# Kernel optimization log

Hardware: AMD Instinct MI355X
Metric: run time of the kernel (lower is better)

The kernel has to match this reference:

```python
import jax, jax.numpy as jnp
import numpy as np

B, T, C, H, DH = 4, 2048, 1024, 16, 64  # batch, seq (block_size), n_embd, heads, head_size


def setup_inputs() -> dict:
    key = jax.random.key(0)
    ks = jax.random.split(key, 6)
    x = jax.random.normal(ks[0], (B, T, C), dtype=jnp.float32)
    init = 0.02
    Wq = jax.random.normal(ks[1], (H, C, DH), dtype=jnp.float32) * init
    Wk = jax.random.normal(ks[2], (H, C, DH), dtype=jnp.float32) * init
    Wv = jax.random.normal(ks[3], (H, C, DH), dtype=jnp.float32) * init
    Wp = jax.random.normal(ks[4], (H * DH, C), dtype=jnp.float32) * init
    bp = jnp.zeros((C,), dtype=jnp.float32)
    return {"x": x, "Wq": Wq, "Wk": Wk, "Wv": Wv, "Wp": Wp, "bp": bp}


def reference(x, Wq, Wk, Wv, Wp, bp):
    Bb, Tt, Cc = x.shape
    # per-head projections, vectorized over heads (original loops in Python)
    q = jnp.einsum('btc,hcd->bhtd', x, Wq)
    k = jnp.einsum('btc,hcd->bhtd', x, Wk)
    v = jnp.einsum('btc,hcd->bhtd', x, Wv)
    # NOTE: original scales by rsqrt(C) where C is the INPUT embed dim, not head_size
    scale = 1.0 / jnp.sqrt(jnp.asarray(Cc, dtype=x.dtype))
    wei = jnp.einsum('bhtd,bhsd->bhts', q, k) * scale  # [B,H,T,T]
    causal = jnp.tril(jnp.ones((Tt, Tt), dtype=bool))
    wei = jnp.where(causal, wei, -jnp.inf)
    wei = jax.nn.softmax(wei, axis=-1)
    out = jnp.einsum('bhts,bhsd->bhtd', wei, v)  # [B,H,T,DH]
    # concat heads along feature axis (head h -> slice h*DH:(h+1)*DH)
    out = out.transpose(0, 2, 1, 3).reshape(Bb, Tt, -1)  # [B,T,H*DH]
    out = out @ Wp + bp  # output projection to n_embd
    return out
```

## Files before the change

kernel.cpp:

```cpp
#include <hip/hip_runtime.h>

#define TSEQ 2048
#define CDIM 1024
#define NH 16
#define DH 64
#define NB 4

typedef __bf16 bf16x8 __attribute__((ext_vector_type(8)));
typedef float f32x4 __attribute__((ext_vector_type(4)));

#define QSCALE 0.04508422f

static __device__ __forceinline__ ushort f2bf(float f) {
  unsigned u = __float_as_uint(f);
  unsigned r = u + 0x7fffu + ((u >> 16) & 1u);
  return (ushort)(r >> 16);
}

static __device__ __forceinline__ uint cvtpk(float lo, float hi) {
  uint r;
  asm("v_cvt_pk_bf16_f32 %0, %1, %2" : "=v"(r) : "v"(lo), "v"(hi));
  return r;
}

static __device__ __forceinline__ void gload_lds16(const void* g, void* ldsbase) {
  __builtin_amdgcn_global_load_lds((const __attribute__((address_space(1))) void*)g,
                                   (__attribute__((address_space(3))) void*)ldsbase,
                                   16, 0, 0);
}

__global__ void cvt_x_kernel(const float4* __restrict__ src, ushort4* __restrict__ dst, int n4) {
  int i = blockIdx.x * blockDim.x + threadIdx.x;
  if (i >= n4) return;
  float4 f = src[i];
  ushort4 o;
  o.x = f2bf(f.x); o.y = f2bf(f.y); o.z = f2bf(f.z); o.w = f2bf(f.w);
  dst[i] = o;
}

__global__ void transpose_cvt_all(const float* __restrict__ Wq, const float* __restrict__ Wk,
                                  const float* __restrict__ Wv, const float* __restrict__ Wp,
                                  ushort* __restrict__ wall, ushort* __restrict__ wpT) {
  __shared__ float tile[32][33];
  const int z = blockIdx.z;
  const float* s; ushort* d; int Cc, c0, r0;
  if (z < 3) {
    const int head = blockIdx.x >> 1;
    s = (z == 0 ? Wq : z == 1 ? Wk : Wv) + (size_t)head * CDIM * DH;
    d = wall + ((size_t)z << 20) + (size_t)head * CDIM * DH;
    Cc = DH; c0 = (blockIdx.x & 1) * 32; r0 = blockIdx.y * 32;
  } else {
    s = Wp; d = wpT; Cc = CDIM; c0 = blockIdx.x * 32; r0 = blockIdx.y * 32;
  }
  const int tx = threadIdx.x, ty = threadIdx.y;
  for (int i = ty; i < 32; i += 8)
    tile[i][tx] = s[(size_t)(r0 + i) * Cc + c0 + tx];
  __syncthreads();
  for (int i = ty; i < 32; i += 8)
    d[(size_t)(c0 + i) * CDIM + r0 + tx] = f2bf(tile[tx][i]);
}

template <int MODE>
__global__ __launch_bounds__(256) void gemm_kernel(
    const ushort* __restrict__ A, const ushort* __restrict__ Bt,
    const float* __restrict__ bp, float* __restrict__ fout,
    ushort* __restrict__ qb, ushort* __restrict__ kb, ushort* __restrict__ vTb) {
  __shared__ ushort lds[16384];
  const int tid = threadIdx.x, w = tid >> 6, l = tid & 63;
  const int nwg = gridDim.x;
  const int bid = blockIdx.x;
  const int wgid = (bid & 7) * (nwg >> 3) + (bid >> 3);
  const int NT = (MODE == 0) ? 24 : 8;
  const int nt = wgid % NT, mt = wgid / NT;
  const int wr = w >> 1, wc = w & 1;
  const int srw = l >> 2;
  const int sck = l & 3;
  const int scol = (sck ^ ((srw >> 1) & 3)) * 8;
  const int g = l >> 4;
  char* ldsb = (char*)lds;

  f32x4 acc[4][4] = {};

  const ushort* Arow = A + ((size_t)mt * 128) * CDIM;
  const ushort* Brow = Bt + ((size_t)nt * 128) * CDIM;

#pragma unroll
  for (int i = 0; i < 4; ++i) {
    int ch = w * 4 + i;
    const ushort* src = (ch < 8) ? Arow + (size_t)(ch * 16 + srw) * CDIM + scol
                                 : Brow + (size_t)((ch - 8) * 16 + srw) * CDIM + scol;
    gload_lds16(src, ldsb + ch * 1024);
  }

  for (int k0 = 0; k0 < CDIM; k0 += 32) {
    const int bsel = (k0 >> 5) & 1;
    char* base = ldsb + bsel * 16384;
    __syncthreads();
    if (k0 + 32 < CDIM) {
      char* nb = ldsb + (bsel ^ 1) * 16384;
#pragma unroll
      for (int i = 0; i < 4; ++i) {
        int ch = w * 4 + i;
        const ushort* src = (ch < 8)
            ? Arow + (size_t)(ch * 16 + srw) * CDIM + k0 + 32 + scol
            : Brow + (size_t)((ch - 8) * 16 + srw) * CDIM + k0 + 32 + scol;
        gload_lds16(src, nb + ch * 1024);
      }
    }
    bf16x8 af[4];
#pragma unroll
    for (int fm = 0; fm < 4; ++fm) {
      int row = wr * 64 + fm * 16 + (l & 15);
      af[fm] = *(const bf16x8*)(base + row * 64 + ((g ^ ((row >> 1) & 3)) << 4));
    }
#pragma unroll
    for (int fn = 0; fn < 4; ++fn) {
      int n = wc * 64 + fn * 16 + (l & 15);
      bf16x8 bfr = *(const bf16x8*)(base + 8192 + n * 64 + ((g ^ ((n >> 1) & 3)) << 4));
#pragma unroll
      for (int fm = 0; fm < 4; ++fm)
        acc[fm][fn] = __builtin_amdgcn_mfma_f32_16x16x32_bf16(af[fm], bfr, acc[fm][fn], 0, 0, 0);
    }
  }

#pragma unroll
  for (int fm = 0; fm < 4; ++fm) {
#pragma unroll
    for (int fn = 0; fn < 4; ++fn) {
      const int gr0 = mt * 128 + wr * 64 + fm * 16 + (l >> 4) * 4;
      const int gc = nt * 128 + wc * 64 + fn * 16 + (l & 15);
      if (MODE == 1) {
        float bias = bp[gc];
#pragma unroll
        for (int r = 0; r < 4; ++r)
          fout[(size_t)(gr0 + r) * CDIM + gc] = acc[fm][fn][r] + bias;
      } else {
        const int sel = gc >> 10, h = (gc >> 6) & 15, d = gc & 63;
        const int bh = (gr0 >> 11) * NH + h, tl = gr0 & 2047;
        if (sel == 2) {
          ushort4 pk;
          pk.x = f2bf(acc[fm][fn][0]); pk.y = f2bf(acc[fm][fn][1]);
          pk.z = f2bf(acc[fm][fn][2]); pk.w = f2bf(acc[fm][fn][3]);
          *(ushort4*)(vTb + ((size_t)bh * DH + d) * TSEQ + tl) = pk;
        } else if (sel == 0) {
#pragma unroll
          for (int r = 0; r < 4; ++r)
            qb[((size_t)bh * TSEQ + tl + r) * DH + d] = f2bf(acc[fm][fn][r] * QSCALE);
        } else {
#pragma unroll
          for (int r = 0; r < 4; ++r)
            kb[((size_t)bh * TSEQ + tl + r) * DH + d] = f2bf(acc[fm][fn][r]);
        }
      }
    }
  }
}

__global__ __launch_bounds__(256, 3) void attn_kernel(
    const ushort* __restrict__ qb, const ushort* __restrict__ kb,
    const ushort* __restrict__ vTb, ushort* __restrict__ aob) {
  __shared__ ushort lds[16384];
  char* ldsb = (char*)lds;
  const int tid = threadIdx.x, w = tid >> 6, l = tid & 63;
  const int id = blockIdx.x;
  const int bh = (id & 7) * 8 + ((id >> 3) & 7);
  const int qt = 15 - (id >> 6);
  const int q0 = qt * 128;
  const int nt = 2 * (qt + 1);
  const int b = bh >> 4, h = bh & 15;
  const int g = l >> 4, q = l & 15;
  const int srow = l >> 3;
  const int scol = (((l & 7) ^ srow) << 3);
  const int adrA = ((l & 16) << 1 | q) << 2;
  const int adrB = adrA + 64;
  const bool hi32 = (l & 32) != 0;

  bf16x8 qf[2][2];
#pragma unroll
  for (int qs = 0; qs < 2; ++qs) {
    const ushort* qrow = qb + ((size_t)bh * TSEQ + q0 + w * 32 + qs * 16 + q) * DH;
    qf[qs][0] = *(const bf16x8*)(qrow + 8 * g);
    qf[qs][1] = *(const bf16x8*)(qrow + 32 + 8 * g);
  }

  float m[2] = {0.f, 0.f}, lsum[2] = {0.f, 0.f};
  f32x4 o[4][2] = {};

#pragma unroll
  for (int i = 0; i < 4; ++i) {
    int ch = w * 4 + i;
    if (ch < 8)
      gload_lds16(kb + ((size_t)bh * TSEQ + ch * 8 + srow) * DH + scol, ldsb + ch * 1024);
    else {
      int d = (ch - 8) * 8 + srow;
      gload_lds16(vTb + ((size_t)bh * DH + d) * TSEQ + scol, ldsb + 16384 + (ch - 8) * 1024);
    }
  }

#pragma unroll 1
  for (int j = 0; j < nt; ++j) {
    __syncthreads();
    const int cbuf = j & 1;
    if (j + 1 < nt) {
      const int kvn = (j + 1) * 64, nb = (j + 1) & 1;
#pragma unroll
      for (int i = 0; i < 4; ++i) {
        int ch = w * 4 + i;
        if (ch < 8)
          gload_lds16(kb + ((size_t)bh * TSEQ + kvn + ch * 8 + srow) * DH + scol,
                      ldsb + nb * 8192 + ch * 1024);
        else {
          int d = (ch - 8) * 8 + srow;
          gload_lds16(vTb + ((size_t)bh * DH + d) * TSEQ + kvn + scol,
                      ldsb + 16384 + nb * 8192 + (ch - 8) * 1024);
        }
      }
    }
    char* Kb = ldsb + cbuf * 8192;
    char* Vb = ldsb + 16384 + cbuf * 8192;

    f32x4 s[4][2] = {};
    __builtin_amdgcn_s_setprio(1);
#pragma unroll
    for (int ks = 0; ks < 2; ++ks)
#pragma unroll
      for (int fn = 0; fn < 4; ++fn) {
        int n = fn * 16 + q;
        int cbb = (ks * 64 + 16 * g) ^ ((n & 7) << 4);
        bf16x8 kf = *(const bf16x8*)(Kb + n * 128 + cbb);
        s[fn][0] = __builtin_amdgcn_mfma_f32_16x16x32_bf16(kf, qf[0][ks], s[fn][0], 0, 0, 0);
        s[fn][1] = __builtin_amdgcn_mfma_f32_16x16x32_bf16(kf, qf[1][ks], s[fn][1], 0, 0, 0);
      }
    __builtin_amdgcn_s_setprio(0);

    if (j >= nt - 2) {
#pragma unroll
      for (int qs = 0; qs < 2; ++qs) {
        int rowloc = q0 + w * 32 + qs * 16 + q - j * 64;
#pragma unroll
        for (int fn = 0; fn < 4; ++fn)
#pragma unroll
          for (int r = 0; r < 4; ++r)
            if (fn * 16 + 4 * g + r > rowloc) s[fn][qs][r] = -1e30f;
      }
    }

    float vmx[2];
#pragma unroll
    for (int qs = 0; qs < 2; ++qs) {
      float v = fmaxf(fmaxf(fmaxf(s[0][qs][0], s[0][qs][1]), fmaxf(s[0][qs][2], s[0][qs][3])),
                      fmaxf(fmaxf(s[1][qs][0], s[1][qs][1]), fmaxf(s[1][qs][2], s[1][qs][3])));
      v = fmaxf(v, fmaxf(fmaxf(fmaxf(s[2][qs][0], s[2][qs][1]), fmaxf(s[2][qs][2], s[2][qs][3])),
                         fmaxf(fmaxf(s[3][qs][0], s[3][qs][1]), fmaxf(s[3][qs][2], s[3][qs][3]))));
      vmx[qs] = v;
    }
    if (__any(fmaxf(vmx[0] - m[0], vmx[1] - m[1]) > 8.f)) {
      float fc[2];
#pragma unroll
      for (int qs = 0; qs < 2; ++qs) {
        float v = vmx[qs];
        v = fmaxf(v, __shfl_xor(v, 16));
        v = fmaxf(v, __shfl_xor(v, 32));
        float mn = fmaxf(m[qs], v);
        fc[qs] = __builtin_amdgcn_exp2f(m[qs] - mn);
        m[qs] = mn; lsum[qs] *= fc[qs];
      }
#pragma unroll
      for (int r = 0; r < 4; ++r) {
        float f0 = __shfl(fc[0], (l & 0x30) | (4 * g + r), 64);
        float f1 = __shfl(fc[1], (l & 0x30) | (4 * g + r), 64);
#pragma unroll
        for (int fn = 0; fn < 4; ++fn) { o[fn][0][r] *= f0; o[fn][1][r] *= f1; }
      }
    }

    uint D[2][4][2];
#pragma unroll
    for (int qs = 0; qs < 2; ++qs) {
      float rs = 0.f;
#pragma unroll
      for (int fn = 0; fn < 4; ++fn) {
        float p0 = __builtin_amdgcn_exp2f(s[fn][qs][0] - m[qs]);
        float p1 = __builtin_amdgcn_exp2f(s[fn][qs][1] - m[qs]);
        float p2 = __builtin_amdgcn_exp2f(s[fn][qs][2] - m[qs]);
        float p3 = __builtin_amdgcn_exp2f(s[fn][qs][3] - m[qs]);
        rs += (p0 + p1) + (p2 + p3);
        D[qs][fn][0] = cvtpk(p0, p1);
        D[qs][fn][1] = cvtpk(p2, p3);
      }
      lsum[qs] += rs;
    }

#pragma unroll
    for (int ksg = 0; ksg < 2; ++ksg) {
      union { uint u[4]; bf16x8 v; } P[2];
#pragma unroll
      for (int qs = 0; qs < 2; ++qs) {
        uint t0a = __builtin_amdgcn_ds_bpermute(adrA, (int)D[qs][2 * ksg][0]);
        uint t0b = __builtin_amdgcn_ds_bpermute(adrA, (int)D[qs][2 * ksg + 1][0]);
        uint t1a = __builtin_amdgcn_ds_bpermute(adrA, (int)D[qs][2 * ksg][1]);
        uint t1b = __builtin_amdgcn_ds_bpermute(adrA, (int)D[qs][2 * ksg + 1][1]);
        uint t2a = __builtin_amdgcn_ds_bpermute(adrB, (int)D[qs][2 * ksg][0]);
        uint t2b = __builtin_amdgcn_ds_bpermute(adrB, (int)D[qs][2 * ksg + 1][0]);
        uint t3a = __builtin_amdgcn_ds_bpermute(adrB, (int)D[qs][2 * ksg][1]);
        uint t3b = __builtin_amdgcn_ds_bpermute(adrB, (int)D[qs][2 * ksg + 1][1]);
        P[qs].u[0] = hi32 ? t0b : t0a;
        P[qs].u[1] = hi32 ? t1b : t1a;
        P[qs].u[2] = hi32 ? t2b : t2a;
        P[qs].u[3] = hi32 ? t3b : t3a;
      }
      __builtin_amdgcn_s_setprio(1);
#pragma unroll
      for (int fn = 0; fn < 4; ++fn) {
        int n = fn * 16 + q;
        int cbb = (ksg * 64 + 16 * g) ^ ((n & 7) << 4);
        bf16x8 vf = *(const bf16x8*)(Vb + n * 128 + cbb);
        o[fn][0] = __builtin_amdgcn_mfma_f32_16x16x32_bf16(P[0].v, vf, o[fn][0], 0, 0, 0);
        o[fn][1] = __builtin_amdgcn_mfma_f32_16x16x32_bf16(P[1].v, vf, o[fn][1], 0, 0, 0);
      }
      __builtin_amdgcn_s_setprio(0);
    }
  }

#pragma unroll
  for (int qs = 0; qs < 2; ++qs) {
    float tot = lsum[qs];
    tot += __shfl_xor(tot, 16);
    tot += __shfl_xor(tot, 32);
    float inv = 1.f / tot;
#pragma unroll
    for (int r = 0; r < 4; ++r) {
      float invq = __shfl(inv, (l & 0x30) | (4 * g + r), 64);
      int t = q0 + w * 32 + qs * 16 + 4 * g + r;
#pragma unroll
      for (int fn = 0; fn < 4; ++fn) {
        int d = fn * 16 + q;
        aob[((size_t)b * TSEQ + t) * (NH * DH) + h * DH + d] = f2bf(o[fn][qs][r] * invq);
      }
    }
  }
}

extern "C" void kernel_launch(void* const* d_in, const int* in_sizes, int n_in,
                              void* d_out, int out_size, void* d_ws, size_t ws_size,
                              hipStream_t stream) {
  (void)in_sizes; (void)n_in; (void)out_size; (void)ws_size;
  const float* x  = (const float*)d_in[0];
  const float* Wq = (const float*)d_in[1];
  const float* Wk = (const float*)d_in[2];
  const float* Wv = (const float*)d_in[3];
  const float* Wp = (const float*)d_in[4];
  const float* bp = (const float*)d_in[5];
  float* out = (float*)d_out;
  char* ws = (char*)d_ws;

  ushort* xb  = (ushort*)(ws);
  ushort* wall = (ushort*)(ws + (16ull << 20));
  ushort* wpT = (ushort*)(ws + (22ull << 20));
  ushort* qb  = (ushort*)(ws + (24ull << 20));
  ushort* kb  = (ushort*)(ws + (40ull << 20));
  ushort* vTb = (ushort*)(ws + (56ull << 20));
  ushort* aob = (ushort*)(ws + (72ull << 20));

  cvt_x_kernel<<<(NB * TSEQ * CDIM / 4 + 255) / 256, 256, 0, stream>>>(
      (const float4*)x, (ushort4*)xb, NB * TSEQ * CDIM / 4);
  transpose_cvt_all<<<dim3(32, 32, 4), dim3(32, 8), 0, stream>>>(Wq, Wk, Wv, Wp, wall, wpT);

  gemm_kernel<0><<<dim3(64 * 24), 256, 0, stream>>>(xb, wall, nullptr, nullptr, qb, kb, vTb);
  attn_kernel<<<dim3(1024), 256, 0, stream>>>(qb, kb, vTb, aob);
  gemm_kernel<1><<<dim3(64 * 8), 256, 0, stream>>>(aob, wpT, bp, out, nullptr, nullptr, nullptr);
}
```

Before: 176.0 us.

## Triple-buffer LDS with explicit vmcnt waits in GEMM and attention kernels

```diff
diff --git a/kernel.cpp b/kernel.cpp
--- a/kernel.cpp
+++ b/kernel.cpp
@@ -65,7 +65,7 @@
     const ushort* __restrict__ A, const ushort* __restrict__ Bt,
     const float* __restrict__ bp, float* __restrict__ fout,
     ushort* __restrict__ qb, ushort* __restrict__ kb, ushort* __restrict__ vTb) {
-  __shared__ ushort lds[16384];
+  __shared__ ushort lds[24576];
   const int tid = threadIdx.x, w = tid >> 6, l = tid & 63;
   const int nwg = gridDim.x;
   const int bid = blockIdx.x;
@@ -91,36 +91,49 @@
                                  : Brow + (size_t)((ch - 8) * 16 + srw) * CDIM + scol;
     gload_lds16(src, ldsb + ch * 1024);
   }
-
+  asm volatile("" ::: "memory");
+#pragma unroll
+  for (int i = 0; i < 4; ++i) {
+    int ch = w * 4 + i;
+    const ushort* src = (ch < 8) ? Arow + (size_t)(ch * 16 + srw) * CDIM + 32 + scol
+                                 : Brow + (size_t)((ch - 8) * 16 + srw) * CDIM + 32 + scol;
+    gload_lds16(src, ldsb + 16384 + ch * 1024);
+  }
+
+  char* bc = ldsb;
+  char* b1 = ldsb + 16384;
+  char* b2 = ldsb + 32768;
+#pragma unroll 1
   for (int k0 = 0; k0 < CDIM; k0 += 32) {
-    const int bsel = (k0 >> 5) & 1;
-    char* base = ldsb + bsel * 16384;
-    __syncthreads();
-    if (k0 + 32 < CDIM) {
-      char* nb = ldsb + (bsel ^ 1) * 16384;
+    if (k0 + 32 < CDIM) asm volatile("s_waitcnt vmcnt(4)" ::: "memory");
+    else                asm volatile("s_waitcnt vmcnt(0)" ::: "memory");
+    __builtin_amdgcn_s_barrier();
+    __builtin_amdgcn_sched_barrier(0);
+    if (k0 + 64 < CDIM) {
 #pragma unroll
       for (int i = 0; i < 4; ++i) {
         int ch = w * 4 + i;
         const ushort* src = (ch < 8)
-            ? Arow + (size_t)(ch * 16 + srw) * CDIM + k0 + 32 + scol
-            : Brow + (size_t)((ch - 8) * 16 + srw) * CDIM + k0 + 32 + scol;
-        gload_lds16(src, nb + ch * 1024);
+            ? Arow + (size_t)(ch * 16 + srw) * CDIM + k0 + 64 + scol
+            : Brow + (size_t)((ch - 8) * 16 + srw) * CDIM + k0 + 64 + scol;
+        gload_lds16(src, b2 + ch * 1024);
       }
     }
     bf16x8 af[4];
 #pragma unroll
     for (int fm = 0; fm < 4; ++fm) {
       int row = wr * 64 + fm * 16 + (l & 15);
-      af[fm] = *(const bf16x8*)(base + row * 64 + ((g ^ ((row >> 1) & 3)) << 4));
+      af[fm] = *(const bf16x8*)(bc + row * 64 + ((g ^ ((row >> 1) & 3)) << 4));
     }
 #pragma unroll
     for (int fn = 0; fn < 4; ++fn) {
       int n = wc * 64 + fn * 16 + (l & 15);
-      bf16x8 bfr = *(const bf16x8*)(base + 8192 + n * 64 + ((g ^ ((n >> 1) & 3)) << 4));
+      bf16x8 bfr = *(const bf16x8*)(bc + 8192 + n * 64 + ((g ^ ((n >> 1) & 3)) << 4));
 #pragma unroll
       for (int fm = 0; fm < 4; ++fm)
         acc[fm][fn] = __builtin_amdgcn_mfma_f32_16x16x32_bf16(af[fm], bfr, acc[fm][fn], 0, 0, 0);
     }
+    char* t = bc; bc = b1; b1 = b2; b2 = t;
   }
 
 #pragma unroll
@@ -159,7 +172,7 @@
 __global__ __launch_bounds__(256, 3) void attn_kernel(
     const ushort* __restrict__ qb, const ushort* __restrict__ kb,
     const ushort* __restrict__ vTb, ushort* __restrict__ aob) {
-  __shared__ ushort lds[16384];
+  __shared__ ushort lds[24576];
   char* ldsb = (char*)lds;
   const int tid = threadIdx.x, w = tid >> 6, l = tid & 63;
   const int id = blockIdx.x;
@@ -193,31 +206,47 @@
       gload_lds16(kb + ((size_t)bh * TSEQ + ch * 8 + srow) * DH + scol, ldsb + ch * 1024);
     else {
       int d = (ch - 8) * 8 + srow;
-      gload_lds16(vTb + ((size_t)bh * DH + d) * TSEQ + scol, ldsb + 16384 + (ch - 8) * 1024);
-    }
-  }
-
+      gload_lds16(vTb + ((size_t)bh * DH + d) * TSEQ + scol, ldsb + 24576 + (ch - 8) * 1024);
+    }
+  }
+  asm volatile("" ::: "memory");
+#pragma unroll
+  for (int i = 0; i < 4; ++i) {
+    int ch = w * 4 + i;
+    if (ch < 8)
+      gload_lds16(kb + ((size_t)bh * TSEQ + 64 + ch * 8 + srow) * DH + scol,
+                  ldsb + 8192 + ch * 1024);
+    else {
+      int d = (ch - 8) * 8 + srow;
+      gload_lds16(vTb + ((size_t)bh * DH + d) * TSEQ + 64 + scol,
+                  ldsb + 24576 + 8192 + (ch - 8) * 1024);
+    }
+  }
+
+  int oc = 0, o1 = 8192, o2 = 16384;
 #pragma unroll 1
   for (int j = 0; j < nt; ++j) {
-    __syncthreads();
-    const int cbuf = j & 1;
-    if (j + 1 < nt) {
-      const int kvn = (j + 1) * 64, nb = (j + 1) & 1;
+    if (j + 1 < nt) asm volatile("s_waitcnt vmcnt(4)" ::: "memory");
+    else            asm volatile("s_waitcnt vmcnt(0)" ::: "memory");
+    __builtin_amdgcn_s_barrier();
+    __builtin_amdgcn_sched_barrier(0);
+    if (j + 2 < nt) {
+      const int kvn = (j + 2) * 64;
 #pragma unroll
       for (int i = 0; i < 4; ++i) {
         int ch = w * 4 + i;
         if (ch < 8)
           gload_lds16(kb + ((size_t)bh * TSEQ + kvn + ch * 8 + srow) * DH + scol,
-                      ldsb + nb * 8192 + ch * 1024);
+                      ldsb + o2 + ch * 1024);
         else {
           int d = (ch - 8) * 8 + srow;
           gload_lds16(vTb + ((size_t)bh * DH + d) * TSEQ + kvn + scol,
-                      ldsb + 16384 + nb * 8192 + (ch - 8) * 1024);
+                      ldsb + 24576 + o2 + (ch - 8) * 1024);
         }
       }
     }
-    char* Kb = ldsb + cbuf * 8192;
-    char* Vb = ldsb + 16384 + cbuf * 8192;
+    char* Kb = ldsb + oc;
+    char* Vb = ldsb + 24576 + oc;
 
     f32x4 s[4][2] = {};
     __builtin_amdgcn_s_setprio(1);
@@ -320,6 +349,7 @@
       }
       __builtin_amdgcn_s_setprio(0);
     }
+    int t = oc; oc = o1; o1 = o2; o2 = t;
   }
 
 #pragma unroll
```

Measured after the change: 182.4 us. +3.7%, slower.

## Replace QKV projection GEMM with 256x256-tile 8-wave triple-buffered kernel

Applied to the files above, without the earlier changes.

```diff
diff --git a/kernel.cpp b/kernel.cpp
--- a/kernel.cpp
+++ b/kernel.cpp
@@ -58,6 +58,138 @@
   __syncthreads();
   for (int i = ty; i < 32; i += 8)
     d[(size_t)(c0 + i) * CDIM + r0 + tx] = f2bf(tile[tx][i]);
+}
+
+__global__ __launch_bounds__(512, 2) void qkv8_kernel(
+    const ushort* __restrict__ A, const ushort* __restrict__ Bt,
+    ushort* __restrict__ qb, ushort* __restrict__ kb, ushort* __restrict__ vTb) {
+  __shared__ ushort lds[49152];
+  char* ldsb = (char*)lds;
+  const int tid = threadIdx.x, w = tid >> 6, l = tid & 63;
+  const int nwg = gridDim.x;
+  const int bid = blockIdx.x;
+  const int wgid = (bid & 7) * (nwg >> 3) + (bid >> 3);
+  const int nt = wgid % 12, mt = wgid / 12;
+  const int wr = w >> 2, wc = w & 3;
+  const int g = l >> 4;
+  const int scc = (l & 3) ^ ((l >> 3) & 3);
+  const int strow = l >> 2;
+
+  f32x4 acc[8][4] = {};
+
+  const ushort* Arow = A + ((size_t)mt * 256) * CDIM;
+  const ushort* Brow = Bt + ((size_t)nt * 256) * CDIM;
+
+#pragma unroll
+  for (int tt = 0; tt < 2; ++tt) {
+    char* sl = ldsb + tt * 32768;
+#pragma unroll
+    for (int i = 0; i < 2; ++i) {
+      int ch = w * 2 + i;
+      gload_lds16(Arow + (size_t)(ch * 16 + strow) * CDIM + tt * 32 + scc * 8, sl + ch * 1024);
+    }
+#pragma unroll
+    for (int i = 0; i < 2; ++i) {
+      int ch = w * 2 + i;
+      gload_lds16(Brow + (size_t)(ch * 16 + strow) * CDIM + tt * 32 + scc * 8,
+                  sl + 16384 + ch * 1024);
+    }
+  }
+  asm volatile("s_waitcnt vmcnt(4)" ::: "memory");
+  __builtin_amdgcn_s_barrier();
+
+  char* sl0 = ldsb;
+  char* sl1 = ldsb + 32768;
+  char* sl2 = ldsb + 65536;
+
+#pragma unroll 1
+  for (int t = 0; t < 32; ++t) {
+    bf16x8 af[4], bf[4];
+#pragma unroll
+    for (int fm = 0; fm < 4; ++fm) {
+      int row = wr * 128 + fm * 16 + (l & 15);
+      af[fm] = *(const bf16x8*)(sl0 + row * 64 + ((g ^ ((row >> 1) & 3)) << 4));
+    }
+#pragma unroll
+    for (int fn = 0; fn < 4; ++fn) {
+      int n = wc * 64 + fn * 16 + (l & 15);
+      bf[fn] = *(const bf16x8*)(sl0 + 16384 + n * 64 + ((g ^ ((n >> 1) & 3)) << 4));
+    }
+    if (t + 2 < 32) {
+#pragma unroll
+      for (int i = 0; i < 2; ++i) {
+        int ch = w * 2 + i;
+        gload_lds16(Arow + (size_t)(ch * 16 + strow) * CDIM + (t + 2) * 32 + scc * 8,
+                    sl2 + ch * 1024);
+      }
+    }
+    __builtin_amdgcn_s_barrier();
+    asm volatile("s_waitcnt lgkmcnt(0)" ::: "memory");
+    __builtin_amdgcn_sched_barrier(0);
+    __builtin_amdgcn_s_setprio(1);
+#pragma unroll
+    for (int fn = 0; fn < 4; ++fn)
+#pragma unroll
+      for (int fm = 0; fm < 4; ++fm)
+        acc[fm][fn] = __builtin_amdgcn_mfma_f32_16x16x32_bf16(af[fm], bf[fn], acc[fm][fn], 0, 0, 0);
+    __builtin_amdgcn_s_setprio(0);
+    __builtin_amdgcn_s_barrier();
+
+    bf16x8 af1[4];
+#pragma unroll
+    for (int fm = 0; fm < 4; ++fm) {
+      int row = wr * 128 + 64 + fm * 16 + (l & 15);
+      af1[fm] = *(const bf16x8*)(sl0 + row * 64 + ((g ^ ((row >> 1) & 3)) << 4));
+    }
+    if (t + 2 < 32) {
+#pragma unroll
+      for (int i = 0; i < 2; ++i) {
+        int ch = w * 2 + i;
+        gload_lds16(Brow + (size_t)(ch * 16 + strow) * CDIM + (t + 2) * 32 + scc * 8,
+                    sl2 + 16384 + ch * 1024);
+      }
+    }
+    if (t < 30)       asm volatile("s_waitcnt vmcnt(4)" ::: "memory");
+    else if (t == 30) asm volatile("s_waitcnt vmcnt(0)" ::: "memory");
+    __builtin_amdgcn_s_barrier();
+    asm volatile("s_waitcnt lgkmcnt(0)" ::: "memory");
+    __builtin_amdgcn_sched_barrier(0);
+    __builtin_amdgcn_s_setprio(1);
+#pragma unroll
+    for (int fn = 0; fn < 4; ++fn)
+#pragma unroll
+      for (int fm = 0; fm < 4; ++fm)
+        acc[4 + fm][fn] = __builtin_amdgcn_mfma_f32_16x16x32_bf16(af1[fm], bf[fn], acc[4 + fm][fn], 0, 0, 0);
+    __builtin_amdgcn_s_setprio(0);
+    __builtin_amdgcn_s_barrier();
+
+    char* tmp = sl0; sl0 = sl1; sl1 = sl2; sl2 = tmp;
+  }
+
+#pragma unroll
+  for (int fm2 = 0; fm2 < 8; ++fm2) {
+#pragma unroll
+    for (int fn = 0; fn < 4; ++fn) {
+      const int gr0 = mt * 256 + wr * 128 + fm2 * 16 + (l >> 4) * 4;
+      const int gc = nt * 256 + wc * 64 + fn * 16 + (l & 15);
+      const int sel = gc >> 10, h = (gc >> 6) & 15, d = gc & 63;
+      const int bh = (gr0 >> 11) * NH + h, tl = gr0 & 2047;
+      if (sel == 2) {
+        ushort4 pk;
+        pk.x = f2bf(acc[fm2][fn][0]); pk.y = f2bf(acc[fm2][fn][1]);
+        pk.z = f2bf(acc[fm2][fn][2]); pk.w = f2bf(acc[fm2][fn][3]);
+        *(ushort4*)(vTb + ((size_t)bh * DH + d) * TSEQ + tl) = pk;
+      } else if (sel == 0) {
+#pragma unroll
+        for (int r = 0; r < 4; ++r)
+          qb[((size_t)bh * TSEQ + tl + r) * DH + d] = f2bf(acc[fm2][fn][r] * QSCALE);
+      } else {
+#pragma unroll
+        for (int r = 0; r < 4; ++r)
+          kb[((size_t)bh * TSEQ + tl + r) * DH + d] = f2bf(acc[fm2][fn][r]);
+      }
+    }
+  }
 }
 
 template <int MODE>
@@ -366,7 +498,7 @@
       (const float4*)x, (ushort4*)xb, NB * TSEQ * CDIM / 4);
   transpose_cvt_all<<<dim3(32, 32, 4), dim3(32, 8), 0, stream>>>(Wq, Wk, Wv, Wp, wall, wpT);
 
-  gemm_kernel<0><<<dim3(64 * 24), 256, 0, stream>>>(xb, wall, nullptr, nullptr, qb, kb, vTb);
+  qkv8_kernel<<<dim3(384), 512, 0, stream>>>(xb, wall, qb, kb, vTb);
   attn_kernel<<<dim3(1024), 256, 0, stream>>>(qb, kb, vTb, aob);
   gemm_kernel<1><<<dim3(64 * 8), 256, 0, stream>>>(aob, wpT, bp, out, nullptr, nullptr, nullptr);
 }
```

Result: no change. 173.8 us (-1.2%).
